# Optimization experiments

Measured on AMD Instinct MI355X. Metric: run time of the kernel, lower is better.

Reference implementation:

```python
import jax, jax.numpy as jnp
import numpy as np

B = 8192
D_IN = 10
H = 1900


def _l2norm_cols(w):
    # tf.nn.l2_normalize(w, dim=0): normalize each column, eps 1e-12
    sq = jnp.sum(w * w, axis=0, keepdims=True)
    return w * jax.lax.rsqrt(jnp.maximum(sq, 1e-12))


def setup_inputs() -> dict:
    key = jax.random.key(0)
    ks = jax.random.split(key, 12)
    return {
        "inputs": jax.random.normal(ks[0], (B, D_IN), jnp.float32),
        "c_prev": jax.random.normal(ks[1], (B, H), jnp.float32),
        "h_prev": jax.random.normal(ks[2], (B, H), jnp.float32),
        "wx": jax.random.normal(ks[3], (D_IN, 4 * H), jnp.float32) * 0.1,
        "wh": jax.random.normal(ks[4], (H, 4 * H), jnp.float32) * 0.1,
        "wmx": jax.random.normal(ks[5], (D_IN, H), jnp.float32) * 0.1,
        "wmh": jax.random.normal(ks[6], (H, H), jnp.float32) * 0.1,
        "b": jax.random.normal(ks[7], (4 * H,), jnp.float32) * 0.1,
        "gx": jax.random.uniform(ks[8], (4 * H,), jnp.float32, 0.5, 1.5),
        "gh": jax.random.uniform(ks[9], (4 * H,), jnp.float32, 0.5, 1.5),
        "gmx": jax.random.uniform(ks[10], (H,), jnp.float32, 0.5, 1.5),
        "gmh": jax.random.uniform(ks[11], (H,), jnp.float32, 0.5, 1.5),
    }


def reference(inputs, c_prev, h_prev, wx, wh, wmx, wmh, b, gx, gh, gmx, gmh):
    # weight-normalized weights (per-column l2 norm * gain)
    wx_n = _l2norm_cols(wx) * gx
    wh_n = _l2norm_cols(wh) * gh
    wmx_n = _l2norm_cols(wmx) * gmx
    wmh_n = _l2norm_cols(wmh) * gmh
    # multiplicative state m: [B, H]
    m = (inputs @ wmx_n) * (h_prev @ wmh_n)
    # gate pre-activations z: [B, 4H]
    z = inputs @ wx_n + m @ wh_n + b
    i, f, o, u = jnp.split(z, 4, axis=1)
    i = jax.nn.sigmoid(i)
    f = jax.nn.sigmoid(f)
    o = jax.nn.sigmoid(o)
    u = jnp.tanh(u)
    c = f * c_prev + i * u
    h = o * jnp.tanh(c)
    return (h, c)
```

## Files before the change

kernel.cpp:

```cpp
#include <hip/hip_runtime.h>

typedef unsigned short ushort_t;
typedef short bf16x8 __attribute__((ext_vector_type(8)));
typedef float f32x4 __attribute__((ext_vector_type(4)));

#define H 1900
#define FH 7600
#define BATCH 8192
#define KP 1952
#define NP_A 1920
#define NB 7680
#define BK 32
#define KITERS (KP / BK)

static const size_t OFF_SWX  = 0;
static const size_t OFF_SWH  = 32768;
static const size_t OFF_SWMX = 65536;
static const size_t OFF_SWMH = 73728;
static const size_t OFF_WMXN = 81920;
static const size_t OFF_PART = 163840;
static const size_t OFF_HBF  = 786432;
static const size_t OFF_MEXT = OFF_HBF + 31981568;
static const size_t OFF_WMHT = OFF_MEXT + 31981568;
static const size_t OFF_WHXT = OFF_WMHT + 7495680;

#define PW_X  0
#define PW_H  60800
#define PW_MX 121600
#define PW_MH 136800

__device__ __forceinline__ ushort_t f2bf(float x) {
  unsigned u = __float_as_uint(x);
  return (ushort_t)((u + 0x7fffu + ((u >> 16) & 1u)) >> 16);
}

__device__ __forceinline__ void gl_lds16(const ushort_t* g, ushort_t* lds) {
  __builtin_amdgcn_global_load_lds(
      (const __attribute__((address_space(1))) unsigned int*)(g),
      (__attribute__((address_space(3))) unsigned int*)(lds), 16, 0, 0);
}

__global__ void colsum_partial_kernel(const float* __restrict__ wx, const float* __restrict__ wh,
                                      const float* __restrict__ wmx, const float* __restrict__ wmh,
                                      float* __restrict__ parts) {
  int c = blockIdx.x * 256 + threadIdx.x;
  int y = blockIdx.y, p = blockIdx.z;
  const float* W; int K, N; float* out;
  if (y == 0)      { W = wx;  K = 10;   N = FH; out = parts + PW_X  + (size_t)p * FH; }
  else if (y == 1) { W = wh;  K = 1900; N = FH; out = parts + PW_H  + (size_t)p * FH; }
  else if (y == 2) { W = wmx; K = 10;   N = H;  out = parts + PW_MX + (size_t)p * H;  }
  else             { W = wmh; K = 1900; N = H;  out = parts + PW_MH + (size_t)p * H;  }
  if (c >= N) return;
  int rp = (K + 7) / 8;
  int r0 = p * rp, r1 = r0 + rp; if (r1 > K) r1 = K;
  float s = 0.f;
  for (int r = r0; r < r1; ++r) { float v = W[(size_t)r * N + c]; s += v * v; }
  out[c] = s;
}

__global__ void scales_final_kernel(const float* __restrict__ parts,
                                    const float* __restrict__ gx, const float* __restrict__ gh,
                                    const float* __restrict__ gmx, const float* __restrict__ gmh,
                                    float* __restrict__ s_wx, float* __restrict__ s_wh,
                                    float* __restrict__ s_wmx, float* __restrict__ s_wmh) {
  int c = blockIdx.x * 256 + threadIdx.x;
  int y = blockIdx.y;
  const float* pp; int N; const float* g; float* out;
  if (y == 0)      { pp = parts + PW_X;  N = FH; g = gx;  out = s_wx;  }
  else if (y == 1) { pp = parts + PW_H;  N = FH; g = gh;  out = s_wh;  }
  else if (y == 2) { pp = parts + PW_MX; N = H;  g = gmx; out = s_wmx; }
  else             { pp = parts + PW_MH; N = H;  g = gmh; out = s_wmh; }
  if (c >= N) return;
  float s = 0.f;
  for (int p = 0; p < 8; ++p) s += pp[(size_t)p * N + c];
  out[c] = g[c] * rsqrtf(fmaxf(s, 1e-12f));
}

__global__ void cvt_h_kernel(const float* __restrict__ h_prev, ushort_t* __restrict__ hbf) {
  size_t idx = (size_t)blockIdx.x * 256 + threadIdx.x;
  int row = (int)(idx / KP), col = (int)(idx % KP);
  float v = (col < H) ? h_prev[(size_t)row * H + col] : 0.f;
  hbf[idx] = f2bf(v);
}

__global__ void wmxn_kernel(const float* __restrict__ wmx, const float* __restrict__ s_wmx,
                            float* __restrict__ wmxn) {
  int idx = blockIdx.x * 256 + threadIdx.x;
  int i = idx / NP_A, j = idx - i * NP_A;
  wmxn[idx] = (j < H) ? wmx[i * H + j] * s_wmx[j] : 0.f;
}

__global__ void wmhT_kernel(const float* __restrict__ wmh, const float* __restrict__ s_wmh,
                            ushort_t* __restrict__ wmhT) {
  __shared__ float tile[32][33];
  int n0 = blockIdx.x * 32, k0 = blockIdx.y * 32;
  int tx = threadIdx.x & 31, ty = threadIdx.x >> 5;
#pragma unroll
  for (int it = 0; it < 4; ++it) {
    int k = k0 + ty + it * 8, n = n0 + tx;
    float v = (k < H && n < H) ? wmh[(size_t)k * H + n] : 0.f;
    tile[ty + it * 8][tx] = v;
  }
  __syncthreads();
#pragma unroll
  for (int it = 0; it < 4; ++it) {
    int n = n0 + ty + it * 8, k = k0 + tx;
    float v = tile[tx][ty + it * 8];
    float s = (n < H) ? s_wmh[n] : 0.f;
    wmhT[(size_t)n * KP + k] = f2bf(v * s);
  }
}

__global__ void whxT_kernel(const float* __restrict__ wh, const float* __restrict__ wx,
                            const float* __restrict__ s_wh, const float* __restrict__ s_wx,
                            ushort_t* __restrict__ whxT) {
  __shared__ float tile[32][33];
  int c0 = blockIdx.x * 32, k0 = blockIdx.y * 32;
  int tx = threadIdx.x & 31, ty = threadIdx.x >> 5;
#pragma unroll
  for (int it = 0; it < 4; ++it) {
    int k = k0 + ty + it * 8, c = c0 + tx;
    float v = 0.f;
    if (c < FH) {
      if (k < H) v = wh[(size_t)k * FH + c] * s_wh[c];
      else if (k >= NP_A && k < NP_A + 10) v = wx[(size_t)(k - NP_A) * FH + c] * s_wx[c];
    }
    tile[ty + it * 8][tx] = v;
  }
  __syncthreads();
#pragma unroll
  for (int it = 0; it < 4; ++it) {
    int c = c0 + ty + it * 8, k = k0 + tx;
    if (c < FH) {
      int g = c / H; int j = c - g * H; int n = 4 * j + g;
      whxT[(size_t)n * KP + k] = f2bf(tile[tx][ty + it * 8]);
    }
  }
}

__global__ void mext_tail_kernel(const float* __restrict__ inputs, ushort_t* __restrict__ m_ext) {
  int idx = blockIdx.x * 256 + threadIdx.x;
  int row = idx >> 5, c = idx & 31;
  float v = (c < 10) ? inputs[(size_t)row * 10 + c] : 0.f;
  m_ext[(size_t)row * KP + NP_A + c] = f2bf(v);
}

__global__ void whxT_tail_kernel(ushort_t* __restrict__ whxT) {
  int idx = blockIdx.x * 256 + threadIdx.x;
  whxT[(size_t)FH * KP + idx] = 0;
}

__device__ __forceinline__ void gemm_tile(const ushort_t* __restrict__ Ag,
                                          const ushort_t* __restrict__ Bg,
                                          int m0, int n0,
                                          ushort_t* As, ushort_t* Bs,
                                          f32x4 acc[4][4]) {
  const int tid = threadIdx.x;
  const int lane = tid & 63;
  const int quad = lane >> 4;
  const int lo = lane & 15;
  const int wave = tid >> 6;
  const int wm = (wave & 1) << 6;
  const int wn = (wave >> 1) << 6;
  const int sw = (lo >> 1) & 3;

  const int cr = lane >> 2;
  const int hg = (lane & 3) ^ ((lane >> 3) & 3);
  const int r0 = wave * 16 + cr;
  const int r1 = 64 + wave * 16 + cr;
  const ushort_t* gA0 = Ag + (size_t)(m0 + r0) * KP + hg * 8;
  const ushort_t* gA1 = Ag + (size_t)(m0 + r1) * KP + hg * 8;
  const ushort_t* gB0 = Bg + (size_t)(n0 + r0) * KP + hg * 8;
  const ushort_t* gB1 = Bg + (size_t)(n0 + r1) * KP + hg * 8;
  ushort_t* lA0 = As + (wave * 16) * BK;
  ushort_t* lA1 = As + (64 + wave * 16) * BK;
  ushort_t* lB0 = Bs + (wave * 16) * BK;
  ushort_t* lB1 = Bs + (64 + wave * 16) * BK;

  for (int kt = 0; kt < KITERS; ++kt) {
    __syncthreads();
    gl_lds16(gA0, lA0);
    gl_lds16(gA1, lA1);
    gl_lds16(gB0, lB0);
    gl_lds16(gB1, lB1);
    __syncthreads();
    bf16x8 af[4], bfv[4];
#pragma unroll
    for (int mf = 0; mf < 4; ++mf)
      af[mf] = *(const bf16x8*)(As + (wm + mf * 16 + lo) * BK + ((quad ^ sw) << 3));
#pragma unroll
    for (int nf = 0; nf < 4; ++nf)
      bfv[nf] = *(const bf16x8*)(Bs + (wn + nf * 16 + lo) * BK + ((quad ^ sw) << 3));
#pragma unroll
    for (int mf = 0; mf < 4; ++mf)
#pragma unroll
      for (int nf = 0; nf < 4; ++nf)
        acc[mf][nf] = __builtin_amdgcn_mfma_f32_16x16x32_bf16(af[mf], bfv[nf], acc[mf][nf], 0, 0, 0);
    gA0 += BK; gA1 += BK; gB0 += BK; gB1 += BK;
  }
}

__global__ void __launch_bounds__(256) gemmA_kernel(const ushort_t* __restrict__ hbf,
                                                    const ushort_t* __restrict__ wmhT,
                                                    const float* __restrict__ inputs,
                                                    const float* __restrict__ wmxn,
                                                    ushort_t* __restrict__ m_ext) {
  __shared__ __align__(16) char smem[16384];
  ushort_t* As = (ushort_t*)smem;
  ushort_t* Bs = (ushort_t*)(smem + 8192);
  f32x4 acc[4][4];
  f32x4 zv = {0.f, 0.f, 0.f, 0.f};
#pragma unroll
  for (int a = 0; a < 4; ++a)
#pragma unroll
    for (int bq = 0; bq < 4; ++bq) acc[a][bq] = zv;
  int m0 = blockIdx.x * 128, n0 = blockIdx.y * 128;
  gemm_tile(hbf, wmhT, m0, n0, As, Bs, acc);
  __syncthreads();
  float* inL  = (float*)smem;
  float* wmxL = (float*)(smem + 5120);
  for (int t = threadIdx.x; t < 1280; t += 256) {
    int r = t / 10, i = t - r * 10;
    inL[t] = inputs[(size_t)(m0 + r) * 10 + i];
  }
  for (int t = threadIdx.x; t < 1280; t += 256) {
    int i = t >> 7, c = t & 127;
    wmxL[t] = wmxn[i * NP_A + n0 + c];
  }
  __syncthreads();
  const int lane = threadIdx.x & 63, quad = lane >> 4, lo = lane & 15;
  const int wave = threadIdx.x >> 6, wm = (wave & 1) << 6, wn = (wave >> 1) << 6;
#pragma unroll
  for (int mf = 0; mf < 4; ++mf)
#pragma unroll
    for (int r = 0; r < 4; ++r) {
      int rl = wm + mf * 16 + quad * 4 + r;
      float inrow[10];
#pragma unroll
      for (int i = 0; i < 10; ++i) inrow[i] = inL[rl * 10 + i];
#pragma unroll
      for (int nf = 0; nf < 4; ++nf) {
        int cl = wn + nf * 16 + lo;
        float mx = 0.f;
#pragma unroll
        for (int i = 0; i < 10; ++i) mx += inrow[i] * wmxL[i * 128 + cl];
        float mv = acc[mf][nf][r] * mx;
        m_ext[(size_t)(m0 + rl) * KP + (n0 + cl)] = f2bf(mv);
      }
    }
}

__global__ void __launch_bounds__(256) gemmB_kernel(const ushort_t* __restrict__ mext,
                                                    const ushort_t* __restrict__ whxT,
                                                    const float* __restrict__ bvec,
                                                    const float* __restrict__ c_prev,
                                                    float* __restrict__ hout,
                                                    float* __restrict__ cout) {
  __shared__ __align__(16) char smem[16384];
  ushort_t* As = (ushort_t*)smem;
  ushort_t* Bs = (ushort_t*)(smem + 8192);
  f32x4 acc[4][4];
  f32x4 zv = {0.f, 0.f, 0.f, 0.f};
#pragma unroll
  for (int a = 0; a < 4; ++a)
#pragma unroll
    for (int bq = 0; bq < 4; ++bq) acc[a][bq] = zv;
  int m0 = blockIdx.x * 128, n0 = blockIdx.y * 128;
  gemm_tile(mext, whxT, m0, n0, As, Bs, acc);
  const int lane = threadIdx.x & 63, quad = lane >> 4, lo = lane & 15;
  const int wave = threadIdx.x >> 6, wm = (wave & 1) << 6, wn = (wave >> 1) << 6;
#pragma unroll
  for (int nf = 0; nf < 4; ++nf) {
    int gn = n0 + wn + nf * 16 + lo;
    int j = gn >> 2, g = gn & 3;
    float bias = (j < H) ? bvec[g * H + j] : 0.f;
#pragma unroll
    for (int mf = 0; mf < 4; ++mf)
#pragma unroll
      for (int r = 0; r < 4; ++r) {
        float zs = acc[mf][nf][r] + bias;
        float v1 = __shfl_xor(zs, 1);
        float v2 = __shfl_xor(zs, 2);
        float v3 = __shfl_xor(v1, 2);
        if (g == r && j < H) {
          float zi, zf, zo, zu;
          { int t = 0 ^ g; zi = t == 0 ? zs : t == 1 ? v1 : t == 2 ? v2 : v3; }
          { int t = 1 ^ g; zf = t == 0 ? zs : t == 1 ? v1 : t == 2 ? v2 : v3; }
          { int t = 2 ^ g; zo = t == 0 ? zs : t == 1 ? v1 : t == 2 ? v2 : v3; }
          { int t = 3 ^ g; zu = t == 0 ? zs : t == 1 ? v1 : t == 2 ? v2 : v3; }
          float iv = 1.f / (1.f + __expf(-zi));
          float fv = 1.f / (1.f + __expf(-zf));
          float ov = 1.f / (1.f + __expf(-zo));
          float uv = tanhf(zu);
          int row = m0 + wm + mf * 16 + quad * 4 + r;
          size_t oidx = (size_t)row * H + j;
          float cp = c_prev[oidx];
          float cv = fv * cp + iv * uv;
          hout[oidx] = ov * tanhf(cv);
          cout[oidx] = cv;
        }
      }
  }
}

extern "C" void kernel_launch(void* const* d_in, const int* in_sizes, int n_in,
                              void* d_out, int out_size, void* d_ws, size_t ws_size,
                              hipStream_t stream) {
  const float* inputs = (const float*)d_in[0];
  const float* c_prev = (const float*)d_in[1];
  const float* h_prev = (const float*)d_in[2];
  const float* wx  = (const float*)d_in[3];
  const float* wh  = (const float*)d_in[4];
  const float* wmx = (const float*)d_in[5];
  const float* wmh = (const float*)d_in[6];
  const float* bv  = (const float*)d_in[7];
  const float* gx  = (const float*)d_in[8];
  const float* gh  = (const float*)d_in[9];
  const float* gmx = (const float*)d_in[10];
  const float* gmh = (const float*)d_in[11];

  char* ws = (char*)d_ws;
  float* s_wx  = (float*)(ws + OFF_SWX);
  float* s_wh  = (float*)(ws + OFF_SWH);
  float* s_wmx = (float*)(ws + OFF_SWMX);
  float* s_wmh = (float*)(ws + OFF_SWMH);
  float* wmxn  = (float*)(ws + OFF_WMXN);
  float* parts = (float*)(ws + OFF_PART);
  ushort_t* hbf   = (ushort_t*)(ws + OFF_HBF);
  ushort_t* m_ext = (ushort_t*)(ws + OFF_MEXT);
  ushort_t* wmhT  = (ushort_t*)(ws + OFF_WMHT);
  ushort_t* whxT  = (ushort_t*)(ws + OFF_WHXT);

  float* hout = (float*)d_out;
  float* cout = hout + (size_t)BATCH * H;

  colsum_partial_kernel<<<dim3(30, 4, 8), 256, 0, stream>>>(wx, wh, wmx, wmh, parts);
  scales_final_kernel<<<dim3(30, 4), 256, 0, stream>>>(parts, gx, gh, gmx, gmh,
                                                       s_wx, s_wh, s_wmx, s_wmh);
  cvt_h_kernel<<<62464, 256, 0, stream>>>(h_prev, hbf);
  wmxn_kernel<<<75, 256, 0, stream>>>(wmx, s_wmx, wmxn);
  wmhT_kernel<<<dim3(60, 61), 256, 0, stream>>>(wmh, s_wmh, wmhT);
  whxT_kernel<<<dim3(238, 61), 256, 0, stream>>>(wh, wx, s_wh, s_wx, whxT);
  mext_tail_kernel<<<1024, 256, 0, stream>>>(inputs, m_ext);
  whxT_tail_kernel<<<610, 256, 0, stream>>>(whxT);
  gemmA_kernel<<<dim3(64, 15), 256, 0, stream>>>(hbf, wmhT, inputs, wmxn, m_ext);
  gemmB_kernel<<<dim3(64, 60), 256, 0, stream>>>(m_ext, whxT, bv, c_prev, hout, cout);
}
```

Measured before the change: 1.086 ms.

## Double GEMM K-tile to 64 and merge small prep kernels into one launch

```diff
diff --git a/kernel.cpp b/kernel.cpp
--- a/kernel.cpp
+++ b/kernel.cpp
@@ -7,10 +7,9 @@
 #define H 1900
 #define FH 7600
 #define BATCH 8192
-#define KP 1952
+#define KP 1984
 #define NP_A 1920
-#define NB 7680
-#define BK 32
+#define BK 64
 #define KITERS (KP / BK)
 
 static const size_t OFF_SWX  = 0;
@@ -20,9 +19,9 @@
 static const size_t OFF_WMXN = 81920;
 static const size_t OFF_PART = 163840;
 static const size_t OFF_HBF  = 786432;
-static const size_t OFF_MEXT = OFF_HBF + 31981568;
-static const size_t OFF_WMHT = OFF_MEXT + 31981568;
-static const size_t OFF_WHXT = OFF_WMHT + 7495680;
+static const size_t OFF_MEXT = OFF_HBF  + 32505856;
+static const size_t OFF_WMHT = OFF_MEXT + 32505856;
+static const size_t OFF_WHXT = OFF_WMHT + 7618560;
 
 #define PW_X  0
 #define PW_H  60800
@@ -77,17 +76,32 @@
 }
 
 __global__ void cvt_h_kernel(const float* __restrict__ h_prev, ushort_t* __restrict__ hbf) {
-  size_t idx = (size_t)blockIdx.x * 256 + threadIdx.x;
-  int row = (int)(idx / KP), col = (int)(idx % KP);
+  int col = blockIdx.x * 256 + threadIdx.x;
+  int row = blockIdx.y;
+  if (col >= KP) return;
   float v = (col < H) ? h_prev[(size_t)row * H + col] : 0.f;
-  hbf[idx] = f2bf(v);
-}
-
-__global__ void wmxn_kernel(const float* __restrict__ wmx, const float* __restrict__ s_wmx,
-                            float* __restrict__ wmxn) {
+  hbf[(size_t)row * KP + col] = f2bf(v);
+}
+
+__global__ void misc_prep_kernel(const float* __restrict__ wmx, const float* __restrict__ s_wmx,
+                                 const float* __restrict__ inputs,
+                                 float* __restrict__ wmxn, ushort_t* __restrict__ m_ext,
+                                 ushort_t* __restrict__ whxT) {
   int idx = blockIdx.x * 256 + threadIdx.x;
-  int i = idx / NP_A, j = idx - i * NP_A;
-  wmxn[idx] = (j < H) ? wmx[i * H + j] * s_wmx[j] : 0.f;
+  int y = blockIdx.y;
+  if (y == 0) {
+    if (idx >= 10 * NP_A) return;
+    int i = idx / NP_A, j = idx - i * NP_A;
+    wmxn[idx] = (j < H) ? wmx[i * H + j] * s_wmx[j] : 0.f;
+  } else if (y == 1) {
+    if (idx >= BATCH * 64) return;
+    int row = idx >> 6, c = idx & 63;
+    float v = (c < 10) ? inputs[(size_t)row * 10 + c] : 0.f;
+    m_ext[(size_t)row * KP + NP_A + c] = f2bf(v);
+  } else {
+    if (idx >= 80 * KP) return;
+    whxT[(size_t)FH * KP + idx] = 0;
+  }
 }
 
 __global__ void wmhT_kernel(const float* __restrict__ wmh, const float* __restrict__ s_wmh,
@@ -136,18 +150,6 @@
       whxT[(size_t)n * KP + k] = f2bf(tile[tx][ty + it * 8]);
     }
   }
-}
-
-__global__ void mext_tail_kernel(const float* __restrict__ inputs, ushort_t* __restrict__ m_ext) {
-  int idx = blockIdx.x * 256 + threadIdx.x;
-  int row = idx >> 5, c = idx & 31;
-  float v = (c < 10) ? inputs[(size_t)row * 10 + c] : 0.f;
-  m_ext[(size_t)row * KP + NP_A + c] = f2bf(v);
-}
-
-__global__ void whxT_tail_kernel(ushort_t* __restrict__ whxT) {
-  int idx = blockIdx.x * 256 + threadIdx.x;
-  whxT[(size_t)FH * KP + idx] = 0;
 }
 
 __device__ __forceinline__ void gemm_tile(const ushort_t* __restrict__ Ag,
@@ -159,44 +161,51 @@
   const int lane = tid & 63;
   const int quad = lane >> 4;
   const int lo = lane & 15;
+  const int l7 = lo & 7;
   const int wave = tid >> 6;
   const int wm = (wave & 1) << 6;
   const int wn = (wave >> 1) << 6;
-  const int sw = (lo >> 1) & 3;
-
-  const int cr = lane >> 2;
-  const int hg = (lane & 3) ^ ((lane >> 3) & 3);
-  const int r0 = wave * 16 + cr;
-  const int r1 = 64 + wave * 16 + cr;
-  const ushort_t* gA0 = Ag + (size_t)(m0 + r0) * KP + hg * 8;
-  const ushort_t* gA1 = Ag + (size_t)(m0 + r1) * KP + hg * 8;
-  const ushort_t* gB0 = Bg + (size_t)(n0 + r0) * KP + hg * 8;
-  const ushort_t* gB1 = Bg + (size_t)(n0 + r1) * KP + hg * 8;
-  ushort_t* lA0 = As + (wave * 16) * BK;
-  ushort_t* lA1 = As + (64 + wave * 16) * BK;
-  ushort_t* lB0 = Bs + (wave * 16) * BK;
-  ushort_t* lB1 = Bs + (64 + wave * 16) * BK;
+
+  const int cr8 = lane >> 3;
+  const int hg  = (lane & 7) ^ cr8;
+  const ushort_t* gA[4]; const ushort_t* gB[4];
+  ushort_t* lA[4]; ushort_t* lB[4];
+#pragma unroll
+  for (int i = 0; i < 4; ++i) {
+    int R = wave * 32 + i * 8;
+    gA[i] = Ag + (size_t)(m0 + R + cr8) * KP + hg * 8;
+    gB[i] = Bg + (size_t)(n0 + R + cr8) * KP + hg * 8;
+    lA[i] = As + R * BK;
+    lB[i] = Bs + R * BK;
+  }
 
   for (int kt = 0; kt < KITERS; ++kt) {
     __syncthreads();
-    gl_lds16(gA0, lA0);
-    gl_lds16(gA1, lA1);
-    gl_lds16(gB0, lB0);
-    gl_lds16(gB1, lB1);
+#pragma unroll
+    for (int i = 0; i < 4; ++i) {
+      gl_lds16(gA[i], lA[i]);
+      gl_lds16(gB[i], lB[i]);
+    }
     __syncthreads();
-    bf16x8 af[4], bfv[4];
-#pragma unroll
-    for (int mf = 0; mf < 4; ++mf)
-      af[mf] = *(const bf16x8*)(As + (wm + mf * 16 + lo) * BK + ((quad ^ sw) << 3));
-#pragma unroll
-    for (int nf = 0; nf < 4; ++nf)
-      bfv[nf] = *(const bf16x8*)(Bs + (wn + nf * 16 + lo) * BK + ((quad ^ sw) << 3));
-#pragma unroll
-    for (int mf = 0; mf < 4; ++mf)
+    bf16x8 af[2][4], bfv[2][4];
+#pragma unroll
+    for (int kk = 0; kk < 2; ++kk) {
+#pragma unroll
+      for (int mf = 0; mf < 4; ++mf)
+        af[kk][mf] = *(const bf16x8*)(As + (wm + mf * 16 + lo) * BK + (((kk * 4 + quad) ^ l7) << 3));
 #pragma unroll
       for (int nf = 0; nf < 4; ++nf)
-        acc[mf][nf] = __builtin_amdgcn_mfma_f32_16x16x32_bf16(af[mf], bfv[nf], acc[mf][nf], 0, 0, 0);
-    gA0 += BK; gA1 += BK; gB0 += BK; gB1 += BK;
+        bfv[kk][nf] = *(const bf16x8*)(Bs + (wn + nf * 16 + lo) * BK + (((kk * 4 + quad) ^ l7) << 3));
+    }
+#pragma unroll
+    for (int kk = 0; kk < 2; ++kk)
+#pragma unroll
+      for (int mf = 0; mf < 4; ++mf)
+#pragma unroll
+        for (int nf = 0; nf < 4; ++nf)
+          acc[mf][nf] = __builtin_amdgcn_mfma_f32_16x16x32_bf16(af[kk][mf], bfv[kk][nf], acc[mf][nf], 0, 0, 0);
+#pragma unroll
+    for (int i = 0; i < 4; ++i) { gA[i] += BK; gB[i] += BK; }
   }
 }
 
@@ -205,9 +214,9 @@
                                                     const float* __restrict__ inputs,
                                                     const float* __restrict__ wmxn,
                                                     ushort_t* __restrict__ m_ext) {
-  __shared__ __align__(16) char smem[16384];
+  __shared__ __align__(16) char smem[32768];
   ushort_t* As = (ushort_t*)smem;
-  ushort_t* Bs = (ushort_t*)(smem + 8192);
+  ushort_t* Bs = (ushort_t*)(smem + 16384);
   f32x4 acc[4][4];
   f32x4 zv = {0.f, 0.f, 0.f, 0.f};
 #pragma unroll
@@ -256,9 +265,9 @@
                                                     const float* __restrict__ c_prev,
                                                     float* __restrict__ hout,
                                                     float* __restrict__ cout) {
-  __shared__ __align__(16) char smem[16384];
+  __shared__ __align__(16) char smem[32768];
   ushort_t* As = (ushort_t*)smem;
-  ushort_t* Bs = (ushort_t*)(smem + 8192);
+  ushort_t* Bs = (ushort_t*)(smem + 16384);
   f32x4 acc[4][4];
   f32x4 zv = {0.f, 0.f, 0.f, 0.f};
 #pragma unroll
@@ -337,12 +346,10 @@
   colsum_partial_kernel<<<dim3(30, 4, 8), 256, 0, stream>>>(wx, wh, wmx, wmh, parts);
   scales_final_kernel<<<dim3(30, 4), 256, 0, stream>>>(parts, gx, gh, gmx, gmh,
                                                        s_wx, s_wh, s_wmx, s_wmh);
-  cvt_h_kernel<<<62464, 256, 0, stream>>>(h_prev, hbf);
-  wmxn_kernel<<<75, 256, 0, stream>>>(wmx, s_wmx, wmxn);
-  wmhT_kernel<<<dim3(60, 61), 256, 0, stream>>>(wmh, s_wmh, wmhT);
-  whxT_kernel<<<dim3(238, 61), 256, 0, stream>>>(wh, wx, s_wh, s_wx, whxT);
-  mext_tail_kernel<<<1024, 256, 0, stream>>>(inputs, m_ext);
-  whxT_tail_kernel<<<610, 256, 0, stream>>>(whxT);
+  cvt_h_kernel<<<dim3(8, 8192), 256, 0, stream>>>(h_prev, hbf);
+  wmhT_kernel<<<dim3(60, 62), 256, 0, stream>>>(wmh, s_wmh, wmhT);
+  whxT_kernel<<<dim3(238, 62), 256, 0, stream>>>(wh, wx, s_wh, s_wx, whxT);
+  misc_prep_kernel<<<dim3(2048, 3), 256, 0, stream>>>(wmx, s_wmx, inputs, wmxn, m_ext, whxT);
   gemmA_kernel<<<dim3(64, 15), 256, 0, stream>>>(hbf, wmhT, inputs, wmxn, m_ext);
   gemmB_kernel<<<dim3(64, 60), 256, 0, stream>>>(m_ext, whxT, bv, c_prev, hout, cout);
 }
```

Measured after the change: 1.118 ms. 2.9% more time.
